# Kernel tuning notes

Hardware: AMD Instinct MI355X
Metric: run time of the kernel (lower is better)

The kernel has to match this reference:

```python
import jax, jax.numpy as jnp
import numpy as np

N = 50000
E = 800000
DIN = 128
DH = 128
DOUT = 10
G = 128  # number of graphs in the batch


def gcn_conv(x, W, b, src, dst, n):
    """PyG GCNConv: self-loops + symmetric normalization + scatter-add."""
    loops = jnp.arange(n, dtype=src.dtype)
    s = jnp.concatenate([src, loops])
    d = jnp.concatenate([dst, loops])
    deg = jax.ops.segment_sum(jnp.ones_like(d, dtype=x.dtype), d, num_segments=n)
    dinv = jax.lax.rsqrt(deg)  # deg >= 1 because of self-loops
    norm = dinv[s] * dinv[d]  # [E+N]
    h = x @ W  # [n, out]
    msg = h[s] * norm[:, None]  # gather + scale
    out = jax.ops.segment_sum(msg, d, num_segments=n)  # scatter-add
    return out + b


def setup_inputs() -> dict:
    key = jax.random.key(0)
    ks = jax.random.split(key, 12)
    x = jax.random.normal(ks[0], (N, DIN), dtype=jnp.float32)
    edge_index = jax.random.randint(ks[1], (2, E), 0, N, dtype=jnp.int64)
    batch = jnp.sort(jax.random.randint(ks[2], (N,), 0, G, dtype=jnp.int64))
    def glorot(k, fan_in, fan_out):
        lim = np.sqrt(6.0 / (fan_in + fan_out)).astype(np.float32)
        return jax.random.uniform(k, (fan_in, fan_out), jnp.float32, -lim, lim)
    W1 = glorot(ks[3], DIN, DH); b1 = jnp.zeros((DH,), jnp.float32)
    W2 = glorot(ks[4], DH, DH); b2 = jnp.zeros((DH,), jnp.float32)
    W3 = glorot(ks[5], DH, DH); b3 = jnp.zeros((DH,), jnp.float32)
    Wl = glorot(ks[6], DH, DOUT); bl = jnp.zeros((DOUT,), jnp.float32)
    return {"x": x, "edge_index": edge_index, "batch": batch,
            "W1": W1, "b1": b1, "W2": W2, "b2": b2, "W3": W3, "b3": b3,
            "Wl": Wl, "bl": bl}


def reference(x, edge_index, batch, W1, b1, W2, b2, W3, b3, Wl, bl):
    src, dst = edge_index[0], edge_index[1]
    h = gcn_conv(x, W1, b1, src, dst, N)
    h = jax.nn.relu(h)  # dropout is identity at inference
    h = gcn_conv(h, W2, b2, src, dst, N)
    h = jax.nn.relu(h)
    h = gcn_conv(h, W3, b3, src, dst, N)
    # global mean pool over graphs
    sums = jax.ops.segment_sum(h, batch, num_segments=G)  # [G, DH]
    cnts = jax.ops.segment_sum(jnp.ones((N,), h.dtype), batch, num_segments=G)
    pooled = sums / jnp.maximum(cnts, 1.0)[:, None]
    logits = pooled @ Wl + bl
    return jax.nn.log_softmax(logits, axis=-1)
```

## Files before the change

### kernel.cpp

```cpp
#include <hip/hip_runtime.h>

#define NN 50000
#define NE 800000
#define DHID 128
#define NGR 128
#define DOUT 10

__device__ __forceinline__ unsigned short f2bf(float f) {
    unsigned u = __float_as_uint(f);
    unsigned r = (u + 0x7FFFu + ((u >> 16) & 1u)) >> 16;
    return (unsigned short)r;
}
__device__ __forceinline__ float bf_lo(unsigned int u) {
    return __uint_as_float(u << 16);
}
__device__ __forceinline__ float bf_hi(unsigned int u) {
    return __uint_as_float(u & 0xffff0000u);
}


__global__ void k_init(int* deg, int* cursor, float* gsum) {
    int i = blockIdx.x * blockDim.x + threadIdx.x;
    if (i < NN) { deg[i] = 1; cursor[i] = 0; }
    if (i < NGR * DHID) gsum[i] = 0.f;
}

__global__ void k_count(const int* __restrict__ dst, int* __restrict__ deg) {
    int e = blockIdx.x * blockDim.x + threadIdx.x;
    if (e < NE) atomicAdd(&deg[dst[e]], 1);
}

__device__ __forceinline__ int padcap(int cnt) { return ((cnt + 7) >> 3) << 3; }

__global__ void k_scanA(const int* __restrict__ deg, float* __restrict__ dinv,
                        int* __restrict__ bsum) {
    __shared__ int sm[256];
    int t = threadIdx.x;
    int i = blockIdx.x * 256 + t;
    int d = (i < NN) ? deg[i] : 1;
    if (i < NN) dinv[i] = rsqrtf((float)d);
    sm[t] = padcap(d - 1);
    __syncthreads();
    for (int o = 128; o > 0; o >>= 1) {
        if (t < o) sm[t] += sm[t + o];
        __syncthreads();
    }
    if (t == 0) bsum[blockIdx.x] = sm[0];
}

__global__ void k_scanB(int* bsum, int nb) {
    __shared__ int sm[256];
    int t = threadIdx.x;
    int v = (t < nb) ? bsum[t] : 0;
    sm[t] = v;
    __syncthreads();
    for (int o = 1; o < 256; o <<= 1) {
        int x = (t >= o) ? sm[t - o] : 0;
        __syncthreads();
        sm[t] += x;
        __syncthreads();
    }
    if (t < nb) bsum[t] = sm[t] - v;
}

__global__ void k_scanC(const int* __restrict__ deg, const int* __restrict__ bsum,
                        int* __restrict__ offs) {
    __shared__ int sm[256];
    int t = threadIdx.x;
    int i = blockIdx.x * 256 + t;
    int c = (i < NN) ? padcap(deg[i] - 1) : 0;
    sm[t] = c;
    __syncthreads();
    for (int o = 1; o < 256; o <<= 1) {
        int x = (t >= o) ? sm[t - o] : 0;
        __syncthreads();
        sm[t] += x;
        __syncthreads();
    }
    if (i < NN) offs[i] = bsum[blockIdx.x] + sm[t] - c;
}

__global__ void k_fill(const int* __restrict__ src, const int* __restrict__ dst,
                       const int* __restrict__ offs, int* __restrict__ cursor,
                       const float* __restrict__ dinv,
                       int2* __restrict__ csr) {
    int e = blockIdx.x * blockDim.x + threadIdx.x;
    if (e >= NE) return;
    int s = src[e], d = dst[e];
    int p = offs[d] + atomicAdd(&cursor[d], 1);
    csr[p] = make_int2(s, __float_as_int(dinv[s] * dinv[d]));
}

__global__ void k_pad(const int* __restrict__ deg, const int* __restrict__ offs,
                      int2* __restrict__ csr) {
    int i = blockIdx.x * blockDim.x + threadIdx.x;
    if (i >= NN) return;
    int cnt = deg[i] - 1;
    int cap = padcap(cnt);
    int base = offs[i];
    for (int p = cnt; p < cap; p++) csr[base + p] = make_int2(0, 0);
}

__global__ __launch_bounds__(256) void k_gemm(const float* __restrict__ X,
                                              const float* __restrict__ W,
                                              unsigned short* __restrict__ Cb) {
    __shared__ float Xs[16][68];
    __shared__ float Ws[16][128];
    int t = threadIdx.x;
    int tx = t & 15, ty = t >> 4;
    int rowBase = blockIdx.x * 64;

    float acc[4][8];
#pragma unroll
    for (int i = 0; i < 4; i++)
#pragma unroll
        for (int j = 0; j < 8; j++) acc[i][j] = 0.f;

    for (int kk = 0; kk < 128; kk += 16) {
        {
            int r = t >> 2, q = t & 3;
            int grow = rowBase + r;
            float4 v = make_float4(0.f, 0.f, 0.f, 0.f);
            if (grow < NN)
                v = *reinterpret_cast<const float4*>(&X[grow * 128 + kk + 4 * q]);
            Xs[4 * q + 0][r] = v.x;
            Xs[4 * q + 1][r] = v.y;
            Xs[4 * q + 2][r] = v.z;
            Xs[4 * q + 3][r] = v.w;
        }
#pragma unroll
        for (int rep = 0; rep < 2; rep++) {
            int idx = t + rep * 256;
            int k = idx >> 5, c4 = idx & 31;
            *reinterpret_cast<float4*>(&Ws[k][4 * c4]) =
                *reinterpret_cast<const float4*>(&W[(kk + k) * 128 + 4 * c4]);
        }
        __syncthreads();
#pragma unroll
        for (int k = 0; k < 16; k++) {
            float4 xv = *reinterpret_cast<const float4*>(&Xs[k][4 * ty]);
            float4 w0 = *reinterpret_cast<const float4*>(&Ws[k][8 * tx]);
            float4 w1 = *reinterpret_cast<const float4*>(&Ws[k][8 * tx + 4]);
            float xa[4] = {xv.x, xv.y, xv.z, xv.w};
            float wa[8] = {w0.x, w0.y, w0.z, w0.w, w1.x, w1.y, w1.z, w1.w};
#pragma unroll
            for (int i = 0; i < 4; i++)
#pragma unroll
                for (int j = 0; j < 8; j++) acc[i][j] += xa[i] * wa[j];
        }
        __syncthreads();
    }
#pragma unroll
    for (int i = 0; i < 4; i++) {
        int grow = rowBase + 4 * ty + i;
        if (grow < NN) {
            uint4 o;
            o.x = (unsigned)f2bf(acc[i][0]) | ((unsigned)f2bf(acc[i][1]) << 16);
            o.y = (unsigned)f2bf(acc[i][2]) | ((unsigned)f2bf(acc[i][3]) << 16);
            o.z = (unsigned)f2bf(acc[i][4]) | ((unsigned)f2bf(acc[i][5]) << 16);
            o.w = (unsigned)f2bf(acc[i][6]) | ((unsigned)f2bf(acc[i][7]) << 16);
            *reinterpret_cast<uint4*>(
                &reinterpret_cast<unsigned int*>(Cb)[(size_t)grow * 64 + 4 * tx]) = o;
        }
    }
}

__global__ __launch_bounds__(256) void k_agg(const unsigned int* __restrict__ feat,
                                             const int2* __restrict__ csr,
                                             const int* __restrict__ offs,
                                             const int* __restrict__ deg,
                                             const float* __restrict__ dinv,
                                             const float* __restrict__ bias,
                                             float* __restrict__ out, int relu,
                                             const int* __restrict__ batch,
                                             float* __restrict__ gsum, int do_pool) {
    int wid = threadIdx.x >> 6;
    int lane = threadIdx.x & 63;
    int node = blockIdx.x * 4 + wid;
    if (node >= NN) return;
    float di = dinv[node];
    unsigned int v = feat[(size_t)node * 64 + lane];
    float w0 = di * di;
    float2 a0 = make_float2(w0 * bf_lo(v), w0 * bf_hi(v));
    float2 a1 = make_float2(0.f, 0.f);
    float2 a2 = make_float2(0.f, 0.f);
    float2 a3 = make_float2(0.f, 0.f);
    int start = offs[node];
    int cap = padcap(deg[node] - 1);

    if (cap > 0) {
        int2 p[8];
#pragma unroll
        for (int j = 0; j < 8; j++) p[j] = csr[start + j];
        for (int e = 0; e < cap; e += 8) {
            unsigned int u[8];
#pragma unroll
            for (int j = 0; j < 8; j++) u[j] = feat[(size_t)p[j].x * 64 + lane];
            int2 pn[8];
            if (e + 8 < cap) {
#pragma unroll
                for (int j = 0; j < 8; j++) pn[j] = csr[start + e + 8 + j];
            }
#pragma unroll
            for (int j = 0; j < 8; j++) {
                float w = __int_as_float(p[j].y);
                float ux = bf_lo(u[j]), uy = bf_hi(u[j]);
                if ((j & 3) == 0) { a0.x += w * ux; a0.y += w * uy; }
                if ((j & 3) == 1) { a1.x += w * ux; a1.y += w * uy; }
                if ((j & 3) == 2) { a2.x += w * ux; a2.y += w * uy; }
                if ((j & 3) == 3) { a3.x += w * ux; a3.y += w * uy; }
            }
            if (e + 8 < cap) {
#pragma unroll
                for (int j = 0; j < 8; j++) p[j] = pn[j];
            }
        }
    }

    float2 acc = make_float2(a0.x + a1.x + a2.x + a3.x, a0.y + a1.y + a2.y + a3.y);
    float2 b = reinterpret_cast<const float2*>(bias)[lane];
    acc.x += b.x;
    acc.y += b.y;
    if (relu) {
        acc.x = fmaxf(acc.x, 0.f);
        acc.y = fmaxf(acc.y, 0.f);
    }
    if (do_pool) {
        int g = batch[node];
        atomicAdd(&gsum[g * DHID + 2 * lane + 0], acc.x);
        atomicAdd(&gsum[g * DHID + 2 * lane + 1], acc.y);
    } else {
        reinterpret_cast<float2*>(out)[(size_t)node * 64 + lane] = acc;
    }
}

__global__ __launch_bounds__(128) void k_head(const float* __restrict__ gsum,
                                              const int* __restrict__ batch,
                                              const float* __restrict__ Wl,
                                              const float* __restrict__ bl,
                                              float* __restrict__ out) {
    __shared__ float pooled[128];
    __shared__ float logits[DOUT];
    int g = blockIdx.x;
    int t = threadIdx.x;
    int lo = 0, hi = NN;
    while (lo < hi) {
        int m = (lo + hi) >> 1;
        if (batch[m] < g) lo = m + 1;
        else hi = m;
    }
    int a = lo, b = NN;
    while (a < b) {
        int m = (a + b) >> 1;
        if (batch[m] < g + 1) a = m + 1;
        else b = m;
    }
    int cnt = a - lo;
    pooled[t] = gsum[g * DHID + t] / (float)max(cnt, 1);
    __syncthreads();
    if (t < DOUT) {
        float acc = bl[t];
        for (int k = 0; k < 128; k++) acc += pooled[k] * Wl[k * DOUT + t];
        logits[t] = acc;
    }
    __syncthreads();
    if (t < DOUT) {
        float m = -1e30f;
        for (int j = 0; j < DOUT; j++) m = fmaxf(m, logits[j]);
        float se = 0.f;
        for (int j = 0; j < DOUT; j++) se += expf(logits[j] - m);
        out[g * DOUT + t] = logits[t] - m - logf(se);
    }
}

extern "C" void kernel_launch(void* const* d_in, const int* in_sizes, int n_in,
                              void* d_out, int out_size, void* d_ws, size_t ws_size,
                              hipStream_t stream) {
    const float* x  = (const float*)d_in[0];
    const int*   ei = (const int*)d_in[1];
    const int* batch = (const int*)d_in[2];
    const float* W1 = (const float*)d_in[3];
    const float* b1 = (const float*)d_in[4];
    const float* W2 = (const float*)d_in[5];
    const float* b2 = (const float*)d_in[6];
    const float* W3 = (const float*)d_in[7];
    const float* b3 = (const float*)d_in[8];
    const float* Wl = (const float*)d_in[9];
    const float* bl = (const float*)d_in[10];
    float* out = (float*)d_out;

    const int* src = ei;
    const int* dst = ei + NE;

    char* ws = (char*)d_ws;
    size_t off = 0;
    auto alloc = [&](size_t bytes) {
        void* p = ws + off;
        off += (bytes + 255) / 256 * 256;
        return p;
    };
    int*   deg     = (int*)alloc(NN * 4);
    int*   cursor  = (int*)alloc(NN * 4);
    float* dinv    = (float*)alloc(NN * 4);
    int*   offs    = (int*)alloc(NN * 4);
    int*   bsum    = (int*)alloc(1024);
    float* gsum    = (float*)alloc(NGR * DHID * 4);
    int2*  csr     = (int2*)alloc((size_t)(NE + 8 * NN) * 8);
    unsigned short* hb = (unsigned short*)alloc((size_t)NN * 128 * 2);
    float* A       = (float*)alloc((size_t)NN * 128 * 4);

    int nb = (NN + 255) / 256;
    k_init<<<nb, 256, 0, stream>>>(deg, cursor, gsum);
    k_count<<<NE / 256, 256, 0, stream>>>(dst, deg);
    k_scanA<<<nb, 256, 0, stream>>>(deg, dinv, bsum);
    k_scanB<<<1, 256, 0, stream>>>(bsum, nb);
    k_scanC<<<nb, 256, 0, stream>>>(deg, bsum, offs);
    k_fill<<<NE / 256, 256, 0, stream>>>(src, dst, offs, cursor, dinv, csr);
    k_pad<<<nb, 256, 0, stream>>>(deg, offs, csr);

    int gB = (NN + 63) / 64;
    const unsigned int* hbu = (const unsigned int*)hb;
    k_gemm<<<gB, 256, 0, stream>>>(x, W1, hb);
    k_agg<<<NN / 4, 256, 0, stream>>>(hbu, csr, offs, deg, dinv, b1, A, 1,
                                      batch, gsum, 0);
    k_gemm<<<gB, 256, 0, stream>>>(A, W2, hb);
    k_agg<<<NN / 4, 256, 0, stream>>>(hbu, csr, offs, deg, dinv, b2, A, 1,
                                      batch, gsum, 0);
    k_gemm<<<gB, 256, 0, stream>>>(A, W3, hb);
    k_agg<<<NN / 4, 256, 0, stream>>>(hbu, csr, offs, deg, dinv, b3, A, 0,
                                      batch, gsum, 1);
    k_head<<<NGR, 128, 0, stream>>>(gsum, batch, Wl, bl, out);
}
```

Measured before the change: 483.6 us.

## Split wavefront into four edge groups with 16-byte feature gathers and LDS-staged CSR

The aggregation kernel now splits each 64-lane wavefront into four 16-lane groups. Each group handles a different edge and loads a full 256-byte bf16 row with uint4 loads, and the four partial sums are combined with xor shuffles at the end. CSR entries for each node are staged in LDS first, and per-node padding drops from 8 to 4 edges to cut wasted padded gathers. This trades more registers and shuffle and LDS traffic for fewer, wider memory transactions and less padding work. Only a quarter of the lanes now do the epilogue stores and atomics.

```diff
diff --git a/kernel.cpp b/kernel.cpp
--- a/kernel.cpp
+++ b/kernel.cpp
@@ -5,6 +5,7 @@
 #define DHID 128
 #define NGR 128
 #define DOUT 10
+#define CSR_LDS_CAP 128
 
 __device__ __forceinline__ unsigned short f2bf(float f) {
     unsigned u = __float_as_uint(f);
@@ -18,6 +19,8 @@
     return __uint_as_float(u & 0xffff0000u);
 }
 
+__device__ __forceinline__ int padcap(int cnt) { return ((cnt + 3) >> 2) << 2; }
+
 
 __global__ void k_init(int* deg, int* cursor, float* gsum) {
     int i = blockIdx.x * blockDim.x + threadIdx.x;
@@ -29,8 +32,6 @@
     int e = blockIdx.x * blockDim.x + threadIdx.x;
     if (e < NE) atomicAdd(&deg[dst[e]], 1);
 }
-
-__device__ __forceinline__ int padcap(int cnt) { return ((cnt + 7) >> 3) << 3; }
 
 __global__ void k_scanA(const int* __restrict__ deg, float* __restrict__ dinv,
                         int* __restrict__ bsum) {
@@ -165,7 +166,7 @@
     }
 }
 
-__global__ __launch_bounds__(256) void k_agg(const unsigned int* __restrict__ feat,
+__global__ __launch_bounds__(256) void k_agg(const uint4* __restrict__ feat,
                                              const int2* __restrict__ csr,
                                              const int* __restrict__ offs,
                                              const int* __restrict__ deg,
@@ -174,63 +175,86 @@
                                              float* __restrict__ out, int relu,
                                              const int* __restrict__ batch,
                                              float* __restrict__ gsum, int do_pool) {
+    __shared__ int2 smCsr[4][CSR_LDS_CAP];
     int wid = threadIdx.x >> 6;
     int lane = threadIdx.x & 63;
     int node = blockIdx.x * 4 + wid;
     if (node >= NN) return;
-    float di = dinv[node];
-    unsigned int v = feat[(size_t)node * 64 + lane];
-    float w0 = di * di;
-    float2 a0 = make_float2(w0 * bf_lo(v), w0 * bf_hi(v));
-    float2 a1 = make_float2(0.f, 0.f);
-    float2 a2 = make_float2(0.f, 0.f);
-    float2 a3 = make_float2(0.f, 0.f);
+    int q = lane >> 4;
+    int sub = lane & 15;
+
     int start = offs[node];
     int cap = padcap(deg[node] - 1);
-
-    if (cap > 0) {
-        int2 p[8];
-#pragma unroll
-        for (int j = 0; j < 8; j++) p[j] = csr[start + j];
-        for (int e = 0; e < cap; e += 8) {
-            unsigned int u[8];
-#pragma unroll
-            for (int j = 0; j < 8; j++) u[j] = feat[(size_t)p[j].x * 64 + lane];
-            int2 pn[8];
-            if (e + 8 < cap) {
-#pragma unroll
-                for (int j = 0; j < 8; j++) pn[j] = csr[start + e + 8 + j];
-            }
-#pragma unroll
-            for (int j = 0; j < 8; j++) {
-                float w = __int_as_float(p[j].y);
-                float ux = bf_lo(u[j]), uy = bf_hi(u[j]);
-                if ((j & 3) == 0) { a0.x += w * ux; a0.y += w * uy; }
-                if ((j & 3) == 1) { a1.x += w * ux; a1.y += w * uy; }
-                if ((j & 3) == 2) { a2.x += w * ux; a2.y += w * uy; }
-                if ((j & 3) == 3) { a3.x += w * ux; a3.y += w * uy; }
-            }
-            if (e + 8 < cap) {
-#pragma unroll
-                for (int j = 0; j < 8; j++) p[j] = pn[j];
-            }
-        }
-    }
-
-    float2 acc = make_float2(a0.x + a1.x + a2.x + a3.x, a0.y + a1.y + a2.y + a3.y);
-    float2 b = reinterpret_cast<const float2*>(bias)[lane];
-    acc.x += b.x;
-    acc.y += b.y;
-    if (relu) {
-        acc.x = fmaxf(acc.x, 0.f);
-        acc.y = fmaxf(acc.y, 0.f);
-    }
-    if (do_pool) {
-        int g = batch[node];
-        atomicAdd(&gsum[g * DHID + 2 * lane + 0], acc.x);
-        atomicAdd(&gsum[g * DHID + 2 * lane + 1], acc.y);
-    } else {
-        reinterpret_cast<float2*>(out)[(size_t)node * 64 + lane] = acc;
+    int capL = min(cap, CSR_LDS_CAP);
+    for (int i = lane; i < capL; i += 64) smCsr[wid][i] = csr[start + i];
+
+    float di = dinv[node];
+    float w0 = (q == 0) ? di * di : 0.f;
+    uint4 sv = feat[(size_t)node * 16 + sub];
+    float a[8];
+    a[0] = w0 * bf_lo(sv.x); a[1] = w0 * bf_hi(sv.x);
+    a[2] = w0 * bf_lo(sv.y); a[3] = w0 * bf_hi(sv.y);
+    a[4] = w0 * bf_lo(sv.z); a[5] = w0 * bf_hi(sv.z);
+    a[6] = w0 * bf_lo(sv.w); a[7] = w0 * bf_hi(sv.w);
+
+#define ACC8(W, U)                                                        \
+    do {                                                                  \
+        a[0] += (W) * bf_lo((U).x); a[1] += (W) * bf_hi((U).x);           \
+        a[2] += (W) * bf_lo((U).y); a[3] += (W) * bf_hi((U).y);           \
+        a[4] += (W) * bf_lo((U).z); a[5] += (W) * bf_hi((U).z);           \
+        a[6] += (W) * bf_lo((U).w); a[7] += (W) * bf_hi((U).w);           \
+    } while (0)
+
+    int e = 0;
+    for (; e + 8 <= capL; e += 8) {
+        int2 r0 = smCsr[wid][e + q];
+        int2 r1 = smCsr[wid][e + 4 + q];
+        uint4 u0 = feat[(size_t)r0.x * 16 + sub];
+        uint4 u1 = feat[(size_t)r1.x * 16 + sub];
+        float wA = __int_as_float(r0.y);
+        float wB = __int_as_float(r1.y);
+        ACC8(wA, u0);
+        ACC8(wB, u1);
+    }
+    if (e < capL) {
+        int2 r0 = smCsr[wid][e + q];
+        uint4 u0 = feat[(size_t)r0.x * 16 + sub];
+        float wA = __int_as_float(r0.y);
+        ACC8(wA, u0);
+    }
+    for (int p4 = capL; p4 < cap; p4 += 4) {
+        int2 r0 = csr[start + p4 + q];
+        uint4 u0 = feat[(size_t)r0.x * 16 + sub];
+        float wA = __int_as_float(r0.y);
+        ACC8(wA, u0);
+    }
+#undef ACC8
+
+#pragma unroll
+    for (int k = 0; k < 8; k++) {
+        a[k] += __shfl_xor(a[k], 16, 64);
+        a[k] += __shfl_xor(a[k], 32, 64);
+    }
+
+    if (q == 0) {
+        const float4* b4 = reinterpret_cast<const float4*>(bias);
+        float4 bl0 = b4[2 * sub], bl1 = b4[2 * sub + 1];
+        a[0] += bl0.x; a[1] += bl0.y; a[2] += bl0.z; a[3] += bl0.w;
+        a[4] += bl1.x; a[5] += bl1.y; a[6] += bl1.z; a[7] += bl1.w;
+        if (relu) {
+#pragma unroll
+            for (int k = 0; k < 8; k++) a[k] = fmaxf(a[k], 0.f);
+        }
+        if (do_pool) {
+            int g = batch[node];
+#pragma unroll
+            for (int k = 0; k < 8; k++)
+                atomicAdd(&gsum[g * DHID + 8 * sub + k], a[k]);
+        } else {
+            float4* o4 = reinterpret_cast<float4*>(out + (size_t)node * 128);
+            o4[2 * sub]     = make_float4(a[0], a[1], a[2], a[3]);
+            o4[2 * sub + 1] = make_float4(a[4], a[5], a[6], a[7]);
+        }
     }
 }
 
@@ -305,7 +329,7 @@
     int*   offs    = (int*)alloc(NN * 4);
     int*   bsum    = (int*)alloc(1024);
     float* gsum    = (float*)alloc(NGR * DHID * 4);
-    int2*  csr     = (int2*)alloc((size_t)(NE + 8 * NN) * 8);
+    int2*  csr     = (int2*)alloc((size_t)(NE + 4 * NN) * 8);
     unsigned short* hb = (unsigned short*)alloc((size_t)NN * 128 * 2);
     float* A       = (float*)alloc((size_t)NN * 128 * 4);
 
@@ -319,15 +343,15 @@
     k_pad<<<nb, 256, 0, stream>>>(deg, offs, csr);
 
     int gB = (NN + 63) / 64;
-    const unsigned int* hbu = (const unsigned int*)hb;
+    const uint4* hb4 = (const uint4*)hb;
     k_gemm<<<gB, 256, 0, stream>>>(x, W1, hb);
-    k_agg<<<NN / 4, 256, 0, stream>>>(hbu, csr, offs, deg, dinv, b1, A, 1,
+    k_agg<<<NN / 4, 256, 0, stream>>>(hb4, csr, offs, deg, dinv, b1, A, 1,
                                       batch, gsum, 0);
     k_gemm<<<gB, 256, 0, stream>>>(A, W2, hb);
-    k_agg<<<NN / 4, 256, 0, stream>>>(hbu, csr, offs, deg, dinv, b2, A, 1,
+    k_agg<<<NN / 4, 256, 0, stream>>>(hb4, csr, offs, deg, dinv, b2, A, 1,
                                       batch, gsum, 0);
     k_gemm<<<gB, 256, 0, stream>>>(A, W3, hb);
-    k_agg<<<NN / 4, 256, 0, stream>>>(hbu, csr, offs, deg, dinv, b3, A, 0,
+    k_agg<<<NN / 4, 256, 0, stream>>>(hb4, csr, offs, deg, dinv, b3, A, 0,
                                       batch, gsum, 1);
     k_head<<<NGR, 128, 0, stream>>>(gsum, batch, Wl, bl, out);
 }
```

After: 751.9 us. 1.55x slower.
